# Kernel optimization log

Measured on AMD Instinct MI355X. Metric: run time of the kernel, lower is better.

## Reference

```python
import jax, jax.numpy as jnp
import numpy as np

D = 1024        # embed_size
F = 4096        # ffn_dim
E = 8           # n_experts
K = 2           # top_k_experts
NS = 1          # n_shared
T = 8192        # tokens


def setup_inputs() -> dict:
    key = jax.random.key(0)
    ks = jax.random.split(key, 12)
    s = lambda *sh: 1.0 / np.sqrt(sh[-2] if len(sh) > 1 else sh[-1])
    inp = {
        "x": jax.random.normal(ks[0], (T, D), jnp.float32),
        "gate_w": jax.random.normal(ks[1], (D, E), jnp.float32) * (1.0 / np.sqrt(D)),
        "gate_b": jnp.zeros((E,), jnp.float32),
        "shared_w1": jax.random.normal(ks[2], (NS, D, 2 * F), jnp.float32) * (1.0 / np.sqrt(D)),
        "shared_b1": jnp.zeros((NS, 2 * F), jnp.float32),
        "shared_w2": jax.random.normal(ks[3], (NS, F, D), jnp.float32) * (1.0 / np.sqrt(F)),
        "shared_b2": jnp.zeros((NS, D), jnp.float32),
        "routed_w1": jax.random.normal(ks[4], (E, D, 2 * F), jnp.float32) * (1.0 / np.sqrt(D)),
        "routed_b1": jnp.zeros((E, 2 * F), jnp.float32),
        "routed_w2": jax.random.normal(ks[5], (E, F, D), jnp.float32) * (1.0 / np.sqrt(F)),
        "routed_b2": jnp.zeros((E, D), jnp.float32),
    }
    return inp


def _expert(x, w1, b1, w2, b2):
    # SwiGLU FFN: w2( silu(a) * b ) where [a, b] = chunk(x @ w1 + b1)
    h = x @ w1 + b1                      # [T, 2F]
    a, b = jnp.split(h, 2, axis=-1)      # [T, F] each
    return (jax.nn.silu(a) * b) @ w2 + b2  # [T, D]


def reference(x, gate_w, gate_b, shared_w1, shared_b1, shared_w2, shared_b2,
              routed_w1, routed_b1, routed_w2, routed_b2):
    # shared experts (always active)
    shared_out = jnp.zeros_like(x)
    for i in range(NS):
        shared_out = shared_out + _expert(x, shared_w1[i], shared_b1[i], shared_w2[i], shared_b2[i])

    # softmax gating + top-k selection
    logits = x @ gate_w + gate_b                      # [T, E]
    probs = jax.nn.softmax(logits, axis=-1)
    topk_probs, topk_idx = jax.lax.top_k(probs, K)    # [T, K]

    # per-token combine weight for each expert: sum_k p_k * 1[idx_k == e]
    one_hot = jax.nn.one_hot(topk_idx, E, dtype=x.dtype)        # [T, K, E]
    combine = jnp.einsum("tk,tke->te", topk_probs, one_hot)     # [T, E]

    # dispatch/combine: dense per-expert FFN, weighted by combine (zero off-route)
    routed_out = jnp.zeros_like(x)
    for e in range(E):
        y = _expert(x, routed_w1[e], routed_b1[e], routed_w2[e], routed_b2[e])
        routed_out = routed_out + y * combine[:, e:e + 1]

    return shared_out + routed_out
```

## Files before the change

### kernel.cpp

```cpp
#include <hip/hip_runtime.h>

#define TOK   8192
#define DD    1024
#define FF    4096
#define EE    8
#define TWOF  8192
#define NSLOT 16384
#define PADT  17408

typedef unsigned short u16;
typedef float  f32x16 __attribute__((ext_vector_type(16)));
typedef __bf16 bf16x8 __attribute__((ext_vector_type(8)));

__device__ __forceinline__ u16 f2b(float f) {
  unsigned u = __builtin_bit_cast(unsigned, f);
  u += 0x7fffu + ((u >> 16) & 1u);
  return (u16)(u >> 16);
}

__device__ __forceinline__ void ldslds16(const void* g, void* l) {
  __builtin_amdgcn_global_load_lds((const __attribute__((address_space(1))) void*)g,
                                   (__attribute__((address_space(3))) void*)l, 16, 0, 0);
}

__global__ void gate_kernel(const float* __restrict__ x, const float* __restrict__ gw,
                            const float* __restrict__ gb, int* __restrict__ counts,
                            int* __restrict__ eidx, int* __restrict__ epos,
                            float* __restrict__ ew) {
  const int wave = threadIdx.x >> 6, lane = threadIdx.x & 63;
  const int t = blockIdx.x * 4 + wave;
  float acc[EE] = {0,0,0,0,0,0,0,0};
  const float* xr = x + (size_t)t * DD;
  for (int d = lane; d < DD; d += 64) {
    float xv = xr[d];
    const float* g = gw + (size_t)d * EE;
#pragma unroll
    for (int e = 0; e < EE; ++e) acc[e] += xv * g[e];
  }
#pragma unroll
  for (int e = 0; e < EE; ++e)
#pragma unroll
    for (int off = 32; off > 0; off >>= 1) acc[e] += __shfl_down(acc[e], off);
  if (lane == 0) {
    float l[EE];
#pragma unroll
    for (int e = 0; e < EE; ++e) l[e] = acc[e] + gb[e];
    int i0 = 0;
    for (int e = 1; e < EE; ++e) if (l[e] > l[i0]) i0 = e;
    int i1 = (i0 == 0) ? 1 : 0;
    for (int e = 0; e < EE; ++e) { if (e == i0) continue; if (l[e] > l[i1]) i1 = e; }
    float m = l[0];
    for (int e = 1; e < EE; ++e) m = fmaxf(m, l[e]);
    float s = 0.f, p[EE];
    for (int e = 0; e < EE; ++e) { p[e] = __expf(l[e] - m); s += p[e]; }
    float w0 = p[i0] / s, w1 = p[i1] / s;
    int p0 = atomicAdd(&counts[i0], 1);
    int p1 = atomicAdd(&counts[i1], 1);
    eidx[2*t] = i0; eidx[2*t+1] = i1;
    epos[2*t] = p0; epos[2*t+1] = p1;
    ew[2*t] = w0;  ew[2*t+1] = w1;
  }
}

__global__ void setup_kernel(const int* __restrict__ counts, int* __restrict__ meta) {
  if (threadIdx.x == 0 && blockIdx.x == 0) {
    int s = 0, tm = 0;
    for (int e = 0; e < EE; ++e) {
      meta[e] = s;
      meta[8 + e] = tm;
      s  += (counts[e] + 127) & ~127;
      tm += (counts[e] + 127) >> 7;
    }
    meta[16] = tm;
  }
}

__global__ void slot_kernel(const int* __restrict__ eidx, const int* __restrict__ epos,
                            const float* __restrict__ ew, const int* __restrict__ meta,
                            int* __restrict__ s2t, float* __restrict__ swt,
                            int* __restrict__ t2s) {
  int i = blockIdx.x * 256 + threadIdx.x;
  int e = eidx[i];
  int slot = meta[e] + epos[i];
  s2t[slot] = i >> 1;
  swt[slot] = ew[i];
  t2s[i] = slot;
}

__global__ void cvtx_kernel(const float* __restrict__ x, u16* __restrict__ xb) {
  int i = blockIdx.x * 256 + threadIdx.x;
  float4 v = ((const float4*)x)[i];
  unsigned lo = (unsigned)f2b(v.x) | ((unsigned)f2b(v.y) << 16);
  unsigned hi = (unsigned)f2b(v.z) | ((unsigned)f2b(v.w) << 16);
  ((uint2*)xb)[i] = make_uint2(lo, hi);
}

__global__ void gather_kernel(const u16* __restrict__ xb, const int* __restrict__ s2t,
                              u16* __restrict__ xg) {
  int i = blockIdx.x * 256 + threadIdx.x;
  int row = i >> 7, c = i & 127;
  int tok = s2t[row];
  ((int4*)xg)[(size_t)row * 128 + c] = ((const int4*)xb)[(size_t)tok * 128 + c];
}

__global__ void wt_kernel(const float* __restrict__ srcS, const float* __restrict__ srcR,
                          u16* __restrict__ dst, int K, int N, int permute) {
  __shared__ float tile[32][33];
  const int seg = blockIdx.z;
  const float* src = (seg == 0) ? srcS : srcR + (size_t)(seg - 1) * K * N;
  const int pc0 = blockIdx.x * 32, k0 = blockIdx.y * 32;
  const int tid = threadIdx.x;
  {
    int kk = tid >> 3, j4 = (tid & 7) << 2;
    const float* srow = src + (size_t)(k0 + kk) * N;
#pragma unroll
    for (int q = 0; q < 4; ++q) {
      int n = pc0 + j4 + q;
      int oc = permute ? (((n >> 6) << 5) + (n & 31) + ((n & 32) ? FF : 0)) : n;
      tile[kk][j4 + q] = srow[oc];
    }
  }
  __syncthreads();
  {
    int pp = tid >> 3, kq = (tid & 7) << 2;
    u16* drow = dst + (size_t)seg * N * K + (size_t)(pc0 + pp) * K + k0 + kq;
#pragma unroll
    for (int q = 0; q < 4; ++q) drow[q] = f2b(tile[kq + q][pp]);
  }
}


__device__ __forceinline__ void kloop32(int niter,
    const char* a0, const char* a1, const char* a2, const char* a3,
    const char* b0, const char* b1, const char* b2, const char* b3,
    u16* As, u16* Bs, int tid, f32x16 (&acc)[2][2]) {
  const int lane = tid & 63, l31 = lane & 31, kg = (lane >> 5) * 16;
  const int wid = tid >> 6, wm = wid >> 1, wn = wid & 1;
  const int C = (l31 & 7) << 4;
  const char* rA[4]; const char* rB[4];
#pragma unroll
  for (int ks = 0; ks < 4; ++ks) {
    const int o = (ks * 32 + kg) ^ C;
    rA[ks] = (const char*)As + (wm * 64 + l31) * 128 + o;
    rB[ks] = (const char*)Bs + (wn * 64 + l31) * 128 + o;
  }
  for (int it = 0; it < niter; ++it) {
    const long long kb = (long long)it * 128;
    ldslds16(a0 + kb, As + tid * 8);
    ldslds16(a1 + kb, As + 2048 + tid * 8);
    ldslds16(a2 + kb, As + 4096 + tid * 8);
    ldslds16(a3 + kb, As + 6144 + tid * 8);
    ldslds16(b0 + kb, Bs + tid * 8);
    ldslds16(b1 + kb, Bs + 2048 + tid * 8);
    ldslds16(b2 + kb, Bs + 4096 + tid * 8);
    ldslds16(b3 + kb, Bs + 6144 + tid * 8);
    __syncthreads();
#pragma unroll
    for (int ks = 0; ks < 4; ++ks) {
      bf16x8 af0 = *(const bf16x8*)(rA[ks]);
      bf16x8 af1 = *(const bf16x8*)(rA[ks] + 4096);
      bf16x8 bq0 = *(const bf16x8*)(rB[ks]);
      bf16x8 bq1 = *(const bf16x8*)(rB[ks] + 4096);
      acc[0][0] = __builtin_amdgcn_mfma_f32_32x32x16_bf16(af0, bq0, acc[0][0], 0, 0, 0);
      acc[0][1] = __builtin_amdgcn_mfma_f32_32x32x16_bf16(af0, bq1, acc[0][1], 0, 0, 0);
      acc[1][0] = __builtin_amdgcn_mfma_f32_32x32x16_bf16(af1, bq0, acc[1][0], 0, 0, 0);
      acc[1][1] = __builtin_amdgcn_mfma_f32_32x32x16_bf16(af1, bq1, acc[1][1], 0, 0, 0);
    }
    __syncthreads();
  }
}

__device__ __forceinline__ bool seg_map(int g, const int* __restrict__ counts,
                                        const int* __restrict__ meta,
                                        int& seg, int& tm, int& rowstart, int& rows) {
  if (g < 64) { seg = 0; tm = g; rowstart = 0; rows = TOK; return true; }
  int gr = g - 64;
  if (gr >= meta[16]) return false;
  int e = 0;
  while (gr >= meta[8 + e + 1]) ++e;
  seg = e + 1; tm = gr - meta[8 + e];
  rowstart = meta[e]; rows = counts[e];
  return true;
}

__global__ __launch_bounds__(256, 4)
void gemm1_kernel(const u16* __restrict__ xb, const u16* __restrict__ xg,
                  const u16* __restrict__ w1t, const float* __restrict__ sb1,
                  const float* __restrict__ rb1, const int* __restrict__ counts,
                  const int* __restrict__ meta, u16* __restrict__ hs) {
  __shared__ __align__(16) u16 As[128 * 64];
  __shared__ __align__(16) u16 Bs[128 * 64];
  const int lin = blockIdx.x + 64 * blockIdx.y;
  const int tn = (lin & 7) * 8 + ((lin >> 3) & 7);
  const int g = lin >> 6;
  int seg, tm, rowstart, rows;
  if (!seg_map(g, counts, meta, seg, tm, rowstart, rows)) return;
  const u16* A = (seg == 0) ? xb : xg;
  const int hsbase = (seg == 0) ? 0 : TOK + rowstart;
  const int tid = threadIdx.x, lane = tid & 63, wid = tid >> 6;
  const int wm = wid >> 1, wn = wid & 1;

  const int srow = tid >> 3;
  const int scol = ((tid & 7) * 16) ^ ((srow & 7) << 4);
  const char* Ac = (const char*)A;
  const char* Bc = (const char*)(w1t + (size_t)seg * TWOF * DD);
  const char* a[4]; const char* b[4];
#pragma unroll
  for (int r = 0; r < 4; ++r) {
    int rg = rowstart + tm * 128 + r * 32 + srow;
    a[r] = Ac + (size_t)rg * (DD * 2) + scol;
    b[r] = Bc + (size_t)(tn * 128 + r * 32 + srow) * (DD * 2) + scol;
  }

  f32x16 acc[2][2] = {};
  kloop32(DD / 64, a[0], a[1], a[2], a[3], b[0], b[1], b[2], b[3],
          As, Bs, tid, acc);

  const int l31 = lane & 31, lg = lane >> 5;
  const int rlim = rows - tm * 128;
  const float* b1 = (seg == 0) ? sb1 : rb1 + (size_t)(seg - 1) * TWOF;
  const int f = (tn * 2 + wn) * 32 + l31;
  const float ba = b1[f], bb = b1[FF + f];
  u16* hbase = hs + (size_t)(hsbase + tm * 128) * FF;
#pragma unroll
  for (int mi = 0; mi < 2; ++mi)
#pragma unroll
    for (int reg = 0; reg < 16; ++reg) {
      int lr = wm * 64 + mi * 32 + (reg & 3) + 8 * (reg >> 2) + 4 * lg;
      if (lr < rlim) {
        float av = acc[mi][0][reg] + ba;
        float bv = acc[mi][1][reg] + bb;
        float sv = av / (1.0f + __expf(-av)) * bv;
        hbase[(size_t)lr * FF + f] = f2b(sv);
      }
    }
}

__global__ __launch_bounds__(256, 4)
void gemm2_kernel(const u16* __restrict__ hs, const u16* __restrict__ w2t,
                  const float* __restrict__ sb2, const float* __restrict__ rb2,
                  const int* __restrict__ counts, const int* __restrict__ meta,
                  float* __restrict__ yo) {
  __shared__ __align__(16) u16 As[128 * 64];
  __shared__ __align__(16) u16 Bs[128 * 64];
  const int tn = blockIdx.x;
  const int g = blockIdx.y;
  int seg, tm, rowstart, rows;
  if (!seg_map(g, counts, meta, seg, tm, rowstart, rows)) return;
  const int hrow0 = (seg == 0) ? 0 : TOK + rowstart;
  const int tid = threadIdx.x, lane = tid & 63, wid = tid >> 6;
  const int wm = wid >> 1, wn = wid & 1;

  const int srow = tid >> 3;
  const int scol = ((tid & 7) * 16) ^ ((srow & 7) << 4);
  const char* Ac = (const char*)hs;
  const char* Bc = (const char*)(w2t + (size_t)seg * DD * FF);
  const char* a[4]; const char* b[4];
#pragma unroll
  for (int r = 0; r < 4; ++r) {
    a[r] = Ac + (size_t)(hrow0 + tm * 128 + r * 32 + srow) * (FF * 2) + scol;
    b[r] = Bc + (size_t)(tn * 128 + r * 32 + srow) * (FF * 2) + scol;
  }

  f32x16 acc[2][2] = {};
  kloop32(FF / 64, a[0], a[1], a[2], a[3], b[0], b[1], b[2], b[3],
          As, Bs, tid, acc);

  const int l31 = lane & 31, lg = lane >> 5;
  const int rlim = rows - tm * 128;
  const float* b2 = (seg == 0) ? sb2 : rb2 + (size_t)(seg - 1) * DD;
  const int c0 = tn * 128 + wn * 64 + l31;
  const float bias0 = b2[c0], bias1 = b2[c0 + 32];
  float* ybase = yo + (size_t)(hrow0 + tm * 128) * DD;
#pragma unroll
  for (int mi = 0; mi < 2; ++mi)
#pragma unroll
    for (int reg = 0; reg < 16; ++reg) {
      int lr = wm * 64 + mi * 32 + (reg & 3) + 8 * (reg >> 2) + 4 * lg;
      if (lr < rlim) {
        float* orow = ybase + (size_t)lr * DD;
        orow[c0]      = acc[mi][0][reg] + bias0;
        orow[c0 + 32] = acc[mi][1][reg] + bias1;
      }
    }
}

__global__ void combine_kernel(const float* __restrict__ yo, const int* __restrict__ t2s,
                               const float* __restrict__ ew, float* __restrict__ out) {
  const int t = blockIdx.x, d = threadIdx.x;
  const float4 a  = ((const float4*)(yo + (size_t)t * DD))[d];
  const int s0 = t2s[2*t], s1 = t2s[2*t+1];
  const float w0 = ew[2*t], w1 = ew[2*t+1];
  const float4 r0 = ((const float4*)(yo + (size_t)(TOK + s0) * DD))[d];
  const float4 r1 = ((const float4*)(yo + (size_t)(TOK + s1) * DD))[d];
  float4 r;
  r.x = a.x + w0 * r0.x + w1 * r1.x;
  r.y = a.y + w0 * r0.y + w1 * r1.y;
  r.z = a.z + w0 * r0.z + w1 * r1.z;
  r.w = a.w + w0 * r0.w + w1 * r1.w;
  ((float4*)(out + (size_t)t * DD))[d] = r;
}

extern "C" void kernel_launch(void* const* d_in, const int* in_sizes, int n_in,
                              void* d_out, int out_size, void* d_ws, size_t ws_size,
                              hipStream_t stream) {
  const float* x   = (const float*)d_in[0];
  const float* gw  = (const float*)d_in[1];
  const float* gb  = (const float*)d_in[2];
  const float* sw1 = (const float*)d_in[3];
  const float* sb1 = (const float*)d_in[4];
  const float* sw2 = (const float*)d_in[5];
  const float* sb2 = (const float*)d_in[6];
  const float* rw1 = (const float*)d_in[7];
  const float* rb1 = (const float*)d_in[8];
  const float* rw2 = (const float*)d_in[9];
  const float* rb2 = (const float*)d_in[10];
  float* out = (float*)d_out;

  char* p = (char*)d_ws;
  auto alloc = [&](size_t bytes) { char* r = p; p += (bytes + 255) & ~(size_t)255; return r; };
  int*   counts = (int*)alloc(EE * 4);
  int*   meta   = (int*)alloc(17 * 4);
  int*   eidx   = (int*)alloc((size_t)2 * TOK * 4);
  int*   epos   = (int*)alloc((size_t)2 * TOK * 4);
  float* ew     = (float*)alloc((size_t)2 * TOK * 4);
  int*   s2t    = (int*)alloc((size_t)PADT * 4);
  float* swt    = (float*)alloc((size_t)PADT * 4);
  int*   t2s    = (int*)alloc((size_t)2 * TOK * 4);
  u16*   xb     = (u16*)alloc((size_t)TOK * DD * 2);
  u16*   xg     = (u16*)alloc((size_t)PADT * DD * 2);
  u16*   w1t    = (u16*)alloc((size_t)9 * TWOF * DD * 2);
  u16*   w2t    = (u16*)alloc((size_t)9 * DD * FF * 2);
  u16*   hs     = (u16*)alloc((size_t)(TOK + PADT + 128) * FF * 2);
  float* yo     = (float*)w1t;

  hipMemsetAsync(counts, 0, EE * 4, stream);
  hipMemsetAsync(s2t, 0, (size_t)PADT * 4, stream);
  gate_kernel<<<TOK / 4, 256, 0, stream>>>(x, gw, gb, counts, eidx, epos, ew);
  setup_kernel<<<1, 64, 0, stream>>>(counts, meta);
  slot_kernel<<<(2 * TOK) / 256, 256, 0, stream>>>(eidx, epos, ew, meta, s2t, swt, t2s);
  cvtx_kernel<<<(TOK * DD / 4) / 256, 256, 0, stream>>>(x, xb);
  gather_kernel<<<PADT / 2, 256, 0, stream>>>(xb, s2t, xg);
  wt_kernel<<<dim3(TWOF / 32, DD / 32, 9), 256, 0, stream>>>(sw1, rw1, w1t, DD, TWOF, 1);
  wt_kernel<<<dim3(DD / 32, FF / 32, 9), 256, 0, stream>>>(sw2, rw2, w2t, FF, DD, 0);
  gemm1_kernel<<<dim3(64, 199), 256, 0, stream>>>(xb, xg, w1t, sb1, rb1, counts, meta, hs);
  gemm2_kernel<<<dim3(8, 199), 256, 0, stream>>>(hs, w2t, sb2, rb2, counts, meta, yo);
  combine_kernel<<<TOK, 256, 0, stream>>>(yo, t2s, ew, out);
}
```

Before: 1.112 ms.

## Use 256x256 GEMM tiles with 512 threads and multi-stage LDS pipeline

Both GEMMs move from 128x128 tiles with 4 waves to 256x256 tiles with 8 waves, each wave computing 128x64. A new core loop triple-buffers A and double-buffers B in 160KB of LDS. Fragment reads are double-buffered in registers and the MFMAs are interleaved with them, with s_setprio around the MFMAs. Expert segments are padded to 256 rows, which raises the padded buffers. The aim is higher arithmetic intensity per LDS/global load and overlap of loads with compute, at the cost of more padding waste, heavy register pressure and lower occupancy.

```diff
diff --git a/kernel.cpp b/kernel.cpp
--- a/kernel.cpp
+++ b/kernel.cpp
@@ -6,7 +6,7 @@
 #define EE    8
 #define TWOF  8192
 #define NSLOT 16384
-#define PADT  17408
+#define PADT  18432
 
 typedef unsigned short u16;
 typedef float  f32x16 __attribute__((ext_vector_type(16)));
@@ -68,8 +68,8 @@
     for (int e = 0; e < EE; ++e) {
       meta[e] = s;
       meta[8 + e] = tm;
-      s  += (counts[e] + 127) & ~127;
-      tm += (counts[e] + 127) >> 7;
+      s  += (counts[e] + 255) & ~255;
+      tm += (counts[e] + 255) >> 8;
     }
     meta[16] = tm;
   }
@@ -130,51 +130,95 @@
 }
 
 
-__device__ __forceinline__ void kloop32(int niter,
-    const char* a0, const char* a1, const char* a2, const char* a3,
-    const char* b0, const char* b1, const char* b2, const char* b3,
-    u16* As, u16* Bs, int tid, f32x16 (&acc)[2][2]) {
-  const int lane = tid & 63, l31 = lane & 31, kg = (lane >> 5) * 16;
-  const int wid = tid >> 6, wm = wid >> 1, wn = wid & 1;
+#define STG_A(SLOT, KOFF) { _Pragma("unroll") for (int s = 0; s < 4; ++s) \
+    ldslds16(gsA[s] + (KOFF), lds + (SLOT)*32768 + s*8192 + tid*16); }
+#define STG_B(SLOT, KOFF) { _Pragma("unroll") for (int s = 0; s < 4; ++s) \
+    ldslds16(gsB[s] + (KOFF), lds + 98304 + (SLOT)*32768 + s*8192 + tid*16); }
+
+#define RD_FRAGS(BK, ASLOT, BSLOT, KC) { \
+  _Pragma("unroll") for (int mf = 0; mf < 4; ++mf) \
+    af[BK][mf] = *(const bf16x8*)(lds + (ASLOT)*32768 + aoff[mf] + (KC)); \
+  _Pragma("unroll") for (int nf = 0; nf < 2; ++nf) \
+    bq[BK][nf] = *(const bf16x8*)(lds + (BSLOT)*32768 + boff[nf] + (KC)); }
+
+#define DO_MFMA(BK) { __builtin_amdgcn_s_setprio(1); \
+  _Pragma("unroll") for (int mf = 0; mf < 4; ++mf) \
+  _Pragma("unroll") for (int nf = 0; nf < 2; ++nf) \
+    acc[mf][nf] = __builtin_amdgcn_mfma_f32_32x32x16_bf16(af[BK][mf], bq[BK][nf], acc[mf][nf], 0, 0, 0); \
+  __builtin_amdgcn_s_setprio(0); }
+
+#define BAR_FENCE() { __builtin_amdgcn_s_barrier(); asm volatile("" ::: "memory"); }
+
+template<int NT>
+__device__ __forceinline__ void core256(
+    const char* Aseg, long long lda, long long arow0,
+    const char* Bseg, long long ldb, long long bcol0,
+    char* lds, int tid, f32x16 (&acc)[4][2]) {
+  const int lane = tid & 63, wid = tid >> 6;
+  const int wm = wid >> 2, wn = wid & 3;
+  const int l31 = lane & 31, kg = (lane >> 5) * 16;
   const int C = (l31 & 7) << 4;
-  const char* rA[4]; const char* rB[4];
-#pragma unroll
-  for (int ks = 0; ks < 4; ++ks) {
-    const int o = (ks * 32 + kg) ^ C;
-    rA[ks] = (const char*)As + (wm * 64 + l31) * 128 + o;
-    rB[ks] = (const char*)Bs + (wn * 64 + l31) * 128 + o;
-  }
-  for (int it = 0; it < niter; ++it) {
-    const long long kb = (long long)it * 128;
-    ldslds16(a0 + kb, As + tid * 8);
-    ldslds16(a1 + kb, As + 2048 + tid * 8);
-    ldslds16(a2 + kb, As + 4096 + tid * 8);
-    ldslds16(a3 + kb, As + 6144 + tid * 8);
-    ldslds16(b0 + kb, Bs + tid * 8);
-    ldslds16(b1 + kb, Bs + 2048 + tid * 8);
-    ldslds16(b2 + kb, Bs + 4096 + tid * 8);
-    ldslds16(b3 + kb, Bs + 6144 + tid * 8);
-    __syncthreads();
-#pragma unroll
-    for (int ks = 0; ks < 4; ++ks) {
-      bf16x8 af0 = *(const bf16x8*)(rA[ks]);
-      bf16x8 af1 = *(const bf16x8*)(rA[ks] + 4096);
-      bf16x8 bq0 = *(const bf16x8*)(rB[ks]);
-      bf16x8 bq1 = *(const bf16x8*)(rB[ks] + 4096);
-      acc[0][0] = __builtin_amdgcn_mfma_f32_32x32x16_bf16(af0, bq0, acc[0][0], 0, 0, 0);
-      acc[0][1] = __builtin_amdgcn_mfma_f32_32x32x16_bf16(af0, bq1, acc[0][1], 0, 0, 0);
-      acc[1][0] = __builtin_amdgcn_mfma_f32_32x32x16_bf16(af1, bq0, acc[1][0], 0, 0, 0);
-      acc[1][1] = __builtin_amdgcn_mfma_f32_32x32x16_bf16(af1, bq1, acc[1][1], 0, 0, 0);
-    }
-    __syncthreads();
+  int kcol[4];
+#pragma unroll
+  for (int ks = 0; ks < 4; ++ks) kcol[ks] = (ks * 32 + kg) ^ C;
+  int aoff[4], boff[2];
+#pragma unroll
+  for (int mf = 0; mf < 4; ++mf) aoff[mf] = (wm * 128 + mf * 32 + l31) * 128;
+#pragma unroll
+  for (int nf = 0; nf < 2; ++nf) boff[nf] = 98304 + (wn * 64 + nf * 32 + l31) * 128;
+
+  const int srow = tid >> 3, schunk = (tid & 7) * 16;
+  const char* gsA[4]; const char* gsB[4];
+#pragma unroll
+  for (int s = 0; s < 4; ++s) {
+    int rloc = s * 64 + srow;
+    int sw = schunk ^ ((rloc & 7) << 4);
+    gsA[s] = Aseg + (arow0 + rloc) * lda + sw;
+    gsB[s] = Bseg + (bcol0 + rloc) * ldb + sw;
+  }
+
+  bf16x8 af[2][4], bq[2][2];
+
+  STG_A(0, 0);
+  STG_B(0, 0);
+  STG_A(1, 128);
+  asm volatile("s_waitcnt vmcnt(4)" ::: "memory");
+  BAR_FENCE();
+  RD_FRAGS(0, 0, 0, kcol[0]);
+
+  int ia = 0, ib = 0;
+  for (int t = 0; t < NT; ++t) {
+    int iaw = ia + 2; if (iaw >= 3) iaw -= 3;
+    const int ibw = ib ^ 1;
+    if (t + 1 < NT) STG_B(ibw, (long long)(t + 1) * 128);
+    if (t + 2 < NT) STG_A(iaw, (long long)(t + 2) * 128);
+
+    RD_FRAGS(1, ia, ib, kcol[1]);
+    DO_MFMA(0);
+    RD_FRAGS(0, ia, ib, kcol[2]);
+    DO_MFMA(1);
+    RD_FRAGS(1, ia, ib, kcol[3]);
+    DO_MFMA(0);
+
+    if (t + 1 < NT) {
+      if (t + 2 < NT) { asm volatile("s_waitcnt vmcnt(4)" ::: "memory"); }
+      else            { asm volatile("s_waitcnt vmcnt(0)" ::: "memory"); }
+      BAR_FENCE();
+      int ian = ia + 1; if (ian >= 3) ian -= 3;
+      RD_FRAGS(0, ian, ibw, kcol[0]);
+      DO_MFMA(1);
+      ia = ian; ib = ibw;
+    } else {
+      DO_MFMA(1);
+    }
   }
 }
 
 __device__ __forceinline__ bool seg_map(int g, const int* __restrict__ counts,
                                         const int* __restrict__ meta,
                                         int& seg, int& tm, int& rowstart, int& rows) {
-  if (g < 64) { seg = 0; tm = g; rowstart = 0; rows = TOK; return true; }
-  int gr = g - 64;
+  if (g < 32) { seg = 0; tm = g; rowstart = 0; rows = TOK; return true; }
+  int gr = g - 32;
   if (gr >= meta[16]) return false;
   int e = 0;
   while (gr >= meta[8 + e + 1]) ++e;
@@ -183,104 +227,81 @@
   return true;
 }
 
-__global__ __launch_bounds__(256, 4)
+__global__ __launch_bounds__(512, 2)
 void gemm1_kernel(const u16* __restrict__ xb, const u16* __restrict__ xg,
                   const u16* __restrict__ w1t, const float* __restrict__ sb1,
                   const float* __restrict__ rb1, const int* __restrict__ counts,
                   const int* __restrict__ meta, u16* __restrict__ hs) {
-  __shared__ __align__(16) u16 As[128 * 64];
-  __shared__ __align__(16) u16 Bs[128 * 64];
-  const int lin = blockIdx.x + 64 * blockIdx.y;
-  const int tn = (lin & 7) * 8 + ((lin >> 3) & 7);
-  const int g = lin >> 6;
+  __shared__ __align__(16) char lds[163840];
+  const int lin = blockIdx.x + 32 * blockIdx.y;
+  const int tn = (lin & 7) * 4 + ((lin >> 3) & 3);
+  const int g = lin >> 5;
   int seg, tm, rowstart, rows;
   if (!seg_map(g, counts, meta, seg, tm, rowstart, rows)) return;
   const u16* A = (seg == 0) ? xb : xg;
   const int hsbase = (seg == 0) ? 0 : TOK + rowstart;
   const int tid = threadIdx.x, lane = tid & 63, wid = tid >> 6;
-  const int wm = wid >> 1, wn = wid & 1;
-
-  const int srow = tid >> 3;
-  const int scol = ((tid & 7) * 16) ^ ((srow & 7) << 4);
-  const char* Ac = (const char*)A;
-  const char* Bc = (const char*)(w1t + (size_t)seg * TWOF * DD);
-  const char* a[4]; const char* b[4];
-#pragma unroll
-  for (int r = 0; r < 4; ++r) {
-    int rg = rowstart + tm * 128 + r * 32 + srow;
-    a[r] = Ac + (size_t)rg * (DD * 2) + scol;
-    b[r] = Bc + (size_t)(tn * 128 + r * 32 + srow) * (DD * 2) + scol;
-  }
-
-  f32x16 acc[2][2] = {};
-  kloop32(DD / 64, a[0], a[1], a[2], a[3], b[0], b[1], b[2], b[3],
-          As, Bs, tid, acc);
+  const int wm = wid >> 2, wn = wid & 3;
+
+  f32x16 acc[4][2] = {};
+  core256<DD / 64>((const char*)A, DD * 2, rowstart + (long long)tm * 256,
+                   (const char*)(w1t + (size_t)seg * TWOF * DD), DD * 2,
+                   (long long)tn * 256, lds, tid, acc);
 
   const int l31 = lane & 31, lg = lane >> 5;
-  const int rlim = rows - tm * 128;
+  const int rlim = rows - tm * 256;
   const float* b1 = (seg == 0) ? sb1 : rb1 + (size_t)(seg - 1) * TWOF;
-  const int f = (tn * 2 + wn) * 32 + l31;
+  const int f = (tn * 4 + wn) * 32 + l31;
   const float ba = b1[f], bb = b1[FF + f];
-  u16* hbase = hs + (size_t)(hsbase + tm * 128) * FF;
-#pragma unroll
-  for (int mi = 0; mi < 2; ++mi)
+  u16* hbase = hs + (size_t)(hsbase + tm * 256) * FF;
+#pragma unroll
+  for (int mf = 0; mf < 4; ++mf)
 #pragma unroll
     for (int reg = 0; reg < 16; ++reg) {
-      int lr = wm * 64 + mi * 32 + (reg & 3) + 8 * (reg >> 2) + 4 * lg;
+      int lr = wm * 128 + mf * 32 + (reg & 3) + 8 * (reg >> 2) + 4 * lg;
       if (lr < rlim) {
-        float av = acc[mi][0][reg] + ba;
-        float bv = acc[mi][1][reg] + bb;
+        float av = acc[mf][0][reg] + ba;
+        float bv = acc[mf][1][reg] + bb;
         float sv = av / (1.0f + __expf(-av)) * bv;
         hbase[(size_t)lr * FF + f] = f2b(sv);
       }
     }
 }
 
-__global__ __launch_bounds__(256, 4)
+__global__ __launch_bounds__(512, 2)
 void gemm2_kernel(const u16* __restrict__ hs, const u16* __restrict__ w2t,
                   const float* __restrict__ sb2, const float* __restrict__ rb2,
                   const int* __restrict__ counts, const int* __restrict__ meta,
                   float* __restrict__ yo) {
-  __shared__ __align__(16) u16 As[128 * 64];
-  __shared__ __align__(16) u16 Bs[128 * 64];
+  __shared__ __align__(16) char lds[163840];
   const int tn = blockIdx.x;
   const int g = blockIdx.y;
   int seg, tm, rowstart, rows;
   if (!seg_map(g, counts, meta, seg, tm, rowstart, rows)) return;
   const int hrow0 = (seg == 0) ? 0 : TOK + rowstart;
   const int tid = threadIdx.x, lane = tid & 63, wid = tid >> 6;
-  const int wm = wid >> 1, wn = wid & 1;
-
-  const int srow = tid >> 3;
-  const int scol = ((tid & 7) * 16) ^ ((srow & 7) << 4);
-  const char* Ac = (const char*)hs;
-  const char* Bc = (const char*)(w2t + (size_t)seg * DD * FF);
-  const char* a[4]; const char* b[4];
-#pragma unroll
-  for (int r = 0; r < 4; ++r) {
-    a[r] = Ac + (size_t)(hrow0 + tm * 128 + r * 32 + srow) * (FF * 2) + scol;
-    b[r] = Bc + (size_t)(tn * 128 + r * 32 + srow) * (FF * 2) + scol;
-  }
-
-  f32x16 acc[2][2] = {};
-  kloop32(FF / 64, a[0], a[1], a[2], a[3], b[0], b[1], b[2], b[3],
-          As, Bs, tid, acc);
+  const int wm = wid >> 2, wn = wid & 3;
+
+  f32x16 acc[4][2] = {};
+  core256<FF / 64>((const char*)hs, FF * 2, hrow0 + (long long)tm * 256,
+                   (const char*)(w2t + (size_t)seg * DD * FF), FF * 2,
+                   (long long)tn * 256, lds, tid, acc);
 
   const int l31 = lane & 31, lg = lane >> 5;
-  const int rlim = rows - tm * 128;
+  const int rlim = rows - tm * 256;
   const float* b2 = (seg == 0) ? sb2 : rb2 + (size_t)(seg - 1) * DD;
-  const int c0 = tn * 128 + wn * 64 + l31;
+  const int c0 = tn * 256 + wn * 64 + l31;
   const float bias0 = b2[c0], bias1 = b2[c0 + 32];
-  float* ybase = yo + (size_t)(hrow0 + tm * 128) * DD;
-#pragma unroll
-  for (int mi = 0; mi < 2; ++mi)
+  float* ybase = yo + (size_t)(hrow0 + tm * 256) * DD;
+#pragma unroll
+  for (int mf = 0; mf < 4; ++mf)
 #pragma unroll
     for (int reg = 0; reg < 16; ++reg) {
-      int lr = wm * 64 + mi * 32 + (reg & 3) + 8 * (reg >> 2) + 4 * lg;
+      int lr = wm * 128 + mf * 32 + (reg & 3) + 8 * (reg >> 2) + 4 * lg;
       if (lr < rlim) {
         float* orow = ybase + (size_t)lr * DD;
-        orow[c0]      = acc[mi][0][reg] + bias0;
-        orow[c0 + 32] = acc[mi][1][reg] + bias1;
+        orow[c0]      = acc[mf][0][reg] + bias0;
+        orow[c0 + 32] = acc[mf][1][reg] + bias1;
       }
     }
 }
@@ -331,7 +352,7 @@
   u16*   xg     = (u16*)alloc((size_t)PADT * DD * 2);
   u16*   w1t    = (u16*)alloc((size_t)9 * TWOF * DD * 2);
   u16*   w2t    = (u16*)alloc((size_t)9 * DD * FF * 2);
-  u16*   hs     = (u16*)alloc((size_t)(TOK + PADT + 128) * FF * 2);
+  u16*   hs     = (u16*)alloc((size_t)(TOK + PADT + 256) * FF * 2);
   float* yo     = (float*)w1t;
 
   hipMemsetAsync(counts, 0, EE * 4, stream);
@@ -343,7 +364,7 @@
   gather_kernel<<<PADT / 2, 256, 0, stream>>>(xb, s2t, xg);
   wt_kernel<<<dim3(TWOF / 32, DD / 32, 9), 256, 0, stream>>>(sw1, rw1, w1t, DD, TWOF, 1);
   wt_kernel<<<dim3(DD / 32, FF / 32, 9), 256, 0, stream>>>(sw2, rw2, w2t, FF, DD, 0);
-  gemm1_kernel<<<dim3(64, 199), 256, 0, stream>>>(xb, xg, w1t, sb1, rb1, counts, meta, hs);
-  gemm2_kernel<<<dim3(8, 199), 256, 0, stream>>>(hs, w2t, sb2, rb2, counts, meta, yo);
+  gemm1_kernel<<<dim3(32, 104), 512, 0, stream>>>(xb, xg, w1t, sb1, rb1, counts, meta, hs);
+  gemm2_kernel<<<dim3(4, 104), 512, 0, stream>>>(hs, w2t, sb2, rb2, counts, meta, yo);
   combine_kernel<<<TOK, 256, 0, stream>>>(yo, t2s, ew, out);
 }
```

New measurement: 1.141 ms. 2.6% more time.
